# Kernel tuning notes

Measured on AMD Instinct MI355X. Metric: run time of the kernel, lower is better.

Reference implementation:

```python
import jax, jax.numpy as jnp
import numpy as np

LAMBDA_ENTROPY = 0.1
LAMBDA_REPULSION = 0.5
LAMBDA_INTER = 0.3
TEMPERATURE = 1.0
EPS = 1e-8


def setup_inputs() -> dict:
    key = jax.random.key(0)
    k1, k2 = jax.random.split(key)
    membership = jax.random.uniform(k1, (16384, 64, 32), dtype=jnp.float32)   # (N,F,K) soft bin assignments
    teacher_preds = jax.random.uniform(k2, (16384, 128), dtype=jnp.float32)   # (N,C)
    return {"membership": membership, "teacher_preds": teacher_preds}


def reference(membership, teacher_preds):
    N, F, K = membership.shape
    # --- weighted centroids per (feature, bin) ---
    bin_mass = membership.sum(axis=0) + EPS                       # (F,K)
    sum_weighted_y = jnp.einsum('nfk,nc->fkc', membership, teacher_preds)  # avoids (N,F,K,C)
    centroids = sum_weighted_y / bin_mass[..., None]              # (F,K,C)
    # --- weighted intra-bin variance: ||y_n - c_fk||^2 expanded, no (N,F,K,C) tensor ---
    y_sq = jnp.sum(teacher_preds * teacher_preds, axis=-1)        # (N,)
    c_sq = jnp.sum(centroids * centroids, axis=-1)                # (F,K)
    cross = jnp.einsum('nc,fkc->nfk', teacher_preds, centroids)   # (N,F,K)
    dist_sq = y_sq[:, None, None] + c_sq[None, :, :] - 2.0 * cross
    weighted_variance = jnp.sum(membership * dist_sq, axis=0) / bin_mass  # (F,K)
    loss_dispersion = weighted_variance.sum()
    # --- bin-occupancy entropy ---
    p_bins = bin_mass / N                                         # (F,K)
    loss_entropy = jnp.sum(p_bins * jnp.log(p_bins + EPS))
    # --- neighbor repulsion between adjacent bin centroids ---
    neighbor_dist = jnp.sum((centroids[:, :-1, :] - centroids[:, 1:, :]) ** 2, axis=-1)  # (F,K-1)
    loss_repulsion = jnp.sum(jnp.exp(-neighbor_dist / TEMPERATURE))
    # --- all-pairs inter-bin dispersion, batched over F (replaces python loop) ---
    dots = jnp.einsum('fkc,fjc->fkj', centroids, centroids)       # (F,K,K)
    pairwise = c_sq[:, :, None] + c_sq[:, None, :] - 2.0 * dots
    triu = jnp.triu(jnp.ones((K, K), dtype=centroids.dtype), k=1)  # strictly upper
    loss_inter = jnp.sum(jnp.exp(-pairwise / TEMPERATURE) * triu) / F
    total = (loss_dispersion
             + LAMBDA_ENTROPY * loss_entropy
             + LAMBDA_REPULSION * loss_repulsion
             + LAMBDA_INTER * loss_inter)
    return total, loss_dispersion, loss_entropy, loss_repulsion, loss_inter
```

## Files before the change

kernel.cpp:

```cpp
#include <hip/hip_runtime.h>
#include <math.h>

#define N_PTS   16384
#define F_DIM   64
#define K_BINS  32
#define C_DIM   128
#define FK      2048
#define NB32    (N_PTS / 32)
#define CW      132
#define EPS_F   1e-8f

typedef _Float16 f16x8 __attribute__((ext_vector_type(8)));
typedef float    f32x4 __attribute__((ext_vector_type(4)));

__global__ __launch_bounds__(256) void build_ybf_k(const float* __restrict__ Y,
                                                   _Float16* __restrict__ Ybf,
                                                   float* __restrict__ accs) {
    __shared__ __align__(16) float Yl[64][132];
    __shared__ float ysql[64];
    const int t  = threadIdx.x;
    if (blockIdx.x == 0 && t < 8) accs[t] = 0.0f;
    const int n0 = blockIdx.x * 64;
    const int nl = t >> 5;
    const int c4 = t & 31;
#pragma unroll
    for (int p = 0; p < 8; ++p) {
        const int n = p * 8 + nl;
        const float4 v = reinterpret_cast<const float4*>(Y + (size_t)(n0 + n) * C_DIM)[c4];
        reinterpret_cast<float4*>(Yl[n])[c4] = v;
        float sq = v.x * v.x + v.y * v.y + v.z * v.z + v.w * v.w;
#pragma unroll
        for (int m = 16; m >= 1; m >>= 1) sq += __shfl_xor(sq, m, 64);
        if (c4 == 0) ysql[n] = sq;
    }
    __syncthreads();
    for (int p = 0; p < 5; ++p) {
        const int s = t + p * 256;
        if (s < 1152) {
            const int nb2  = s / 576;
            const int r    = s % 576;
            const int ct   = r >> 6;
            const int l    = r & 63;
            const int quad = l >> 4, cl = l & 15;
            const int nloc = nb2 * 32 + quad * 8;
            f16x8 v;
            if (ct < 8) {
                const int c = ct * 16 + cl;
#pragma unroll
                for (int j = 0; j < 8; ++j) v[j] = (_Float16)Yl[nloc + j][c];
            } else if (cl == 0) {
#pragma unroll
                for (int j = 0; j < 8; ++j) v[j] = (_Float16)ysql[nloc + j];
            } else if (cl == 1) {
#pragma unroll
                for (int j = 0; j < 8; ++j) v[j] = (_Float16)1.0f;
            } else {
#pragma unroll
                for (int j = 0; j < 8; ++j) v[j] = (_Float16)0.0f;
            }
            const int nb = blockIdx.x * 2 + nb2;
            *reinterpret_cast<f16x8*>(Ybf + ((size_t)(ct * NB32 + nb) * 64 + l) * 8) = v;
        }
    }
}

__global__ __launch_bounds__(256) void gemm_k(const float* __restrict__ M,
                                              const _Float16* __restrict__ Ybf,
                                              float* __restrict__ wpart,
                                              int cn) {
    __shared__ __align__(16) float    At[2][2][32][32];
    __shared__ __align__(16) _Float16 Bb[2][2][9][512];
    const int t    = threadIdx.x;
    const int fk0  = blockIdx.x * 32;
    const int ch   = blockIdx.y;
    const int w    = t >> 6;
    const int g    = w >> 1;
    const int wl   = w & 1;
    const int l    = t & 63;
    const int quad = l >> 4;
    const int cl   = l & 15;
    const int n0   = ch * cn + g * (cn >> 1);
    const int nb0  = n0 >> 5;
    const int steps = cn >> 6;

    f32x4 acc[9] = {};

#define STAGE(s, par)                                                          \
    {                                                                          \
        const int nb_ = nb0 + (s);                                             \
        _Pragma("unroll")                                                      \
        for (int ct = wl; ct < 9; ct += 2) {                                   \
            const _Float16* g_ = Ybf + ((size_t)(ct * NB32 + nb_) * 64 + l) * 8; \
            __builtin_amdgcn_global_load_lds(                                  \
                (const __attribute__((address_space(1))) unsigned*)g_,         \
                (__attribute__((address_space(3))) unsigned*)&Bb[g][par][ct][0], \
                16, 0, 0);                                                     \
        }                                                                      \
        _Pragma("unroll")                                                      \
        for (int ii = 0; ii < 2; ++ii) {                                       \
            const int i = wl * 2 + ii;                                         \
            const float* gA = M + (size_t)(n0 + (s) * 32 + i * 8 + (l >> 3)) * FK \
                              + fk0 + (l & 7) * 4;                             \
            __builtin_amdgcn_global_load_lds(                                  \
                (const __attribute__((address_space(1))) unsigned*)gA,         \
                (__attribute__((address_space(3))) unsigned*)&At[g][par][i * 8][0], \
                16, 0, 0);                                                     \
        }                                                                      \
    }

    STAGE(0, 0);
    STAGE(1, 1);

    for (int s = 0; s < steps; s += 2) {
        __syncthreads();
        {
            f16x8 bf[9];
#pragma unroll
            for (int ct = 0; ct < 9; ++ct)
                bf[ct] = *reinterpret_cast<const f16x8*>(&Bb[g][0][ct][l * 8]);
            f16x8 af;
#pragma unroll
            for (int j = 0; j < 8; ++j)
                af[j] = (_Float16)At[g][0][quad * 8 + j][wl * 16 + cl];
            __syncthreads();
            if (s + 2 < steps) STAGE(s + 2, 0);
#pragma unroll
            for (int ct = 0; ct < 9; ++ct)
                acc[ct] = __builtin_amdgcn_mfma_f32_16x16x32_f16(af, bf[ct], acc[ct], 0, 0, 0);
        }
        __syncthreads();
        {
            f16x8 bf[9];
#pragma unroll
            for (int ct = 0; ct < 9; ++ct)
                bf[ct] = *reinterpret_cast<const f16x8*>(&Bb[g][1][ct][l * 8]);
            f16x8 af;
#pragma unroll
            for (int j = 0; j < 8; ++j)
                af[j] = (_Float16)At[g][1][quad * 8 + j][wl * 16 + cl];
            __syncthreads();
            if (s + 3 < steps) STAGE(s + 3, 1);
#pragma unroll
            for (int ct = 0; ct < 9; ++ct)
                acc[ct] = __builtin_amdgcn_mfma_f32_16x16x32_f16(af, bf[ct], acc[ct], 0, 0, 0);
        }
    }
#undef STAGE

    float* scr = reinterpret_cast<float*>(&Bb[0][0][0][0]);
    if (g == 1) {
#pragma unroll
        for (int ct = 0; ct < 9; ++ct)
#pragma unroll
            for (int r = 0; r < 4; ++r)
                scr[(wl * 16 + quad * 4 + r) * 144 + ct * 16 + cl] = acc[ct][r];
    }
    __syncthreads();
    if (g == 0) {
        float* wp = wpart + (size_t)ch * FK * CW;
#pragma unroll
        for (int ct = 0; ct < 9; ++ct) {
            const int c = ct * 16 + cl;
            if (c < CW) {
#pragma unroll
                for (int r = 0; r < 4; ++r) {
                    const int row = wl * 16 + quad * 4 + r;
                    const int fk  = fk0 + row;
                    wp[(size_t)fk * CW + c] = acc[ct][r] + scr[row * 144 + c];
                }
            }
        }
    }
}

__global__ __launch_bounds__(128) void reduce_w_k(const float* __restrict__ wpart,
                                                  float* __restrict__ W, int nchunk) {
    const int idx = blockIdx.x * 128 + threadIdx.x;
    const float4* src = reinterpret_cast<const float4*>(wpart);
    const size_t cs = (size_t)FK * CW / 4;
    float4 s0 = make_float4(0.f, 0.f, 0.f, 0.f), s1 = s0, s2 = s0, s3 = s0;
    int ch = 0;
    for (; ch + 3 < nchunk; ch += 4) {
        const float4 a = src[idx + (size_t)(ch + 0) * cs];
        const float4 b = src[idx + (size_t)(ch + 1) * cs];
        const float4 c = src[idx + (size_t)(ch + 2) * cs];
        const float4 d = src[idx + (size_t)(ch + 3) * cs];
        s0.x += a.x; s0.y += a.y; s0.z += a.z; s0.w += a.w;
        s1.x += b.x; s1.y += b.y; s1.z += b.z; s1.w += b.w;
        s2.x += c.x; s2.y += c.y; s2.z += c.z; s2.w += c.w;
        s3.x += d.x; s3.y += d.y; s3.z += d.z; s3.w += d.w;
    }
    for (; ch < nchunk; ++ch) {
        const float4 a = src[idx + (size_t)ch * cs];
        s0.x += a.x; s0.y += a.y; s0.z += a.z; s0.w += a.w;
    }
    float4 r;
    r.x = (s0.x + s1.x) + (s2.x + s3.x);
    r.y = (s0.y + s1.y) + (s2.y + s3.y);
    r.z = (s0.z + s1.z) + (s2.z + s3.z);
    r.w = (s0.w + s1.w) + (s2.w + s3.w);
    reinterpret_cast<float4*>(W)[idx] = r;
}

__global__ __launch_bounds__(256) void epilogue_k(const float* __restrict__ W,
                                                  float* __restrict__ accs,
                                                  float* __restrict__ out) {
    __shared__ __align__(16) float Wl[32][CW];
    __shared__ float Bv[32], Binv[32], S1v[32], csq[32];
    __shared__ float scr[32][8];
    __shared__ float4 red4[256];
    const int t = threadIdx.x;
    const int f = blockIdx.x;

    for (int e = t; e < 32 * 33; e += 256) {
        const int k = e / 33, c4 = e % 33;
        reinterpret_cast<float4*>(Wl[k])[c4] =
            reinterpret_cast<const float4*>(W + (size_t)(f * 32 + k) * CW)[c4];
    }
    __syncthreads();
    if (t < 32) {
        const float B = Wl[t][129] + EPS_F;
        Bv[t] = B; Binv[t] = 1.0f / B; S1v[t] = Wl[t][128];
    }
    __syncthreads();
    {
        const int k = t >> 3, g = t & 7;
        const float ib = Binv[k];
        float s = 0.f;
        for (int c = g * 16; c < g * 16 + 16; ++c) {
            const float v = Wl[k][c] * ib;
            Wl[k][c] = v;
            s = fmaf(v, v, s);
        }
        scr[k][g] = s;
    }
    __syncthreads();
    if (t < 32) {
        float s = 0.f;
#pragma unroll
        for (int g = 0; g < 8; ++g) s += scr[t][g];
        csq[t] = s;
    }
    __syncthreads();

    float my_disp = 0.f, my_ent = 0.f, my_rep = 0.f, my_inter = 0.f;
    if (t < 32) {
        my_disp = (S1v[t] - csq[t] * (Bv[t] + EPS_F)) * Binv[t];
        const float p = Bv[t] * (1.0f / (float)N_PTS);
        my_ent = p * logf(p + EPS_F);
    }
    {
        const int pr = t >> 3, g = t & 7;
        float s = 0.f;
        if (pr < 31) {
            for (int c = g * 16; c < g * 16 + 16; ++c) {
                const float d = Wl[pr][c] - Wl[pr + 1][c];
                s = fmaf(d, d, s);
            }
        }
        __syncthreads();
        scr[pr][g] = s;
    }
    __syncthreads();
    if (t < 31) {
        float d = 0.f;
#pragma unroll
        for (int g = 0; g < 8; ++g) d += scr[t][g];
        my_rep = expf(-d);
    }
#pragma unroll
    for (int s4 = 0; s4 < 4; ++s4) {
        const int slot = t + s4 * 256;
        const int k = slot >> 5, j = slot & 31;
        if (k < j) {
            float dot = 0.f;
            for (int c4 = 0; c4 < 32; ++c4) {
                const float4 a = reinterpret_cast<const float4*>(Wl[k])[c4];
                const float4 b = reinterpret_cast<const float4*>(Wl[j])[c4];
                dot = fmaf(a.x, b.x, dot); dot = fmaf(a.y, b.y, dot);
                dot = fmaf(a.z, b.z, dot); dot = fmaf(a.w, b.w, dot);
            }
            my_inter += expf(-(csq[k] + csq[j] - 2.0f * dot));
        }
    }
    red4[t] = make_float4(my_disp, my_ent, my_rep, my_inter);
    __syncthreads();
    for (int off = 128; off >= 1; off >>= 1) {
        if (t < off) {
            const float4 a = red4[t], b = red4[t + off];
            red4[t] = make_float4(a.x + b.x, a.y + b.y, a.z + b.z, a.w + b.w);
        }
        __syncthreads();
    }
    if (t == 0) {
        atomicAdd(accs + 0, red4[0].x);
        atomicAdd(accs + 1, red4[0].y);
        atomicAdd(accs + 2, red4[0].z);
        atomicAdd(accs + 3, red4[0].w);
        __threadfence();
        const unsigned prev = __hip_atomic_fetch_add(
            reinterpret_cast<unsigned*>(accs + 4), 1u,
            __ATOMIC_ACQ_REL, __HIP_MEMORY_SCOPE_AGENT);
        if (prev == (unsigned)(F_DIM - 1)) {
            const float disp = __hip_atomic_load(accs + 0, __ATOMIC_RELAXED, __HIP_MEMORY_SCOPE_AGENT);
            const float ent  = __hip_atomic_load(accs + 1, __ATOMIC_RELAXED, __HIP_MEMORY_SCOPE_AGENT);
            const float rep  = __hip_atomic_load(accs + 2, __ATOMIC_RELAXED, __HIP_MEMORY_SCOPE_AGENT);
            const float inter = __hip_atomic_load(accs + 3, __ATOMIC_RELAXED, __HIP_MEMORY_SCOPE_AGENT)
                                * (1.0f / (float)F_DIM);
            out[0] = disp + 0.1f * ent + 0.5f * rep + 0.3f * inter;
            out[1] = disp;
            out[2] = ent;
            out[3] = rep;
            out[4] = inter;
        }
    }
}

extern "C" void kernel_launch(void* const* d_in, const int* in_sizes, int n_in,
                              void* d_out, int out_size, void* d_ws, size_t ws_size,
                              hipStream_t stream) {
    const float* M = (const float*)d_in[0];
    const float* Y = (const float*)d_in[1];
    float* out = (float*)d_out;
    char*  ws  = (char*)d_ws;

    const size_t ybfBytes = (size_t)9 * NB32 * 64 * 8 * sizeof(_Float16);
    const size_t wBytes   = (size_t)FK * CW * sizeof(float);

    _Float16* Ybf   = (_Float16*)ws;
    float*    W     = (float*)(ws + ybfBytes);
    float*    accs  = (float*)(ws + ybfBytes + wBytes);
    float*    wpart = (float*)(ws + ybfBytes + wBytes + 1024);

    const size_t used = ybfBytes + wBytes + 1024;
    int nchunk = 16;
    while (nchunk > 1 && used + (size_t)nchunk * wBytes > ws_size) nchunk >>= 1;
    const int cn = N_PTS / nchunk;

    build_ybf_k<<<dim3(N_PTS / 64), dim3(256), 0, stream>>>(Y, Ybf, accs);
    gemm_k<<<dim3(64, nchunk), dim3(256), 0, stream>>>(M, Ybf, wpart, cn);
    reduce_w_k<<<dim3(FK * CW / 4 / 128), dim3(128), 0, stream>>>(wpart, W, nchunk);
    epilogue_k<<<dim3(F_DIM), dim3(256), 0, stream>>>(W, accs, out);
}
```

Baseline: 237.7 us.

## Pre-transpose membership into fp16 MFMA fragment layout in a separate kernel

Adds a build_mt_k pass that reads the fp32 membership tensor once, converts it to fp16 and stores it in the per-lane MFMA A-fragment order. The GEMM then loads A fragments straight into registers with one 16-byte load instead of staging fp32 tiles in LDS and converting per element. The cost is an extra full pass over M (128MB read plus 64MB fp16 write) and 64MB more workspace. The gain depends on whether the GEMM was bound by LDS conversion rather than HBM bandwidth.

Result: slower. 253.0 us (+6.4%).

```diff
diff --git a/kernel.cpp b/kernel.cpp
--- a/kernel.cpp
+++ b/kernel.cpp
@@ -64,11 +64,47 @@
     }
 }
 
-__global__ __launch_bounds__(256) void gemm_k(const float* __restrict__ M,
+__global__ __launch_bounds__(256) void build_mt_k(const float* __restrict__ M,
+                                                  _Float16* __restrict__ Mt) {
+    __shared__ __align__(16) float Lt[32][260];
+    const int t    = threadIdx.x;
+    const int nb   = blockIdx.x;
+    const int half = blockIdx.y;
+    const int n0   = nb * 32;
+#pragma unroll
+    for (int pass = 0; pass < 4; ++pass) {
+        const int fkbase = (half * 4 + pass) * 256;
+        __syncthreads();
+#pragma unroll
+        for (int i = 0; i < 8; ++i) {
+            const int idx = t + i * 256;
+            const int row = idx >> 6;
+            const int c4  = idx & 63;
+            const float4 v = reinterpret_cast<const float4*>(
+                M + (size_t)(n0 + row) * FK + fkbase)[c4];
+            reinterpret_cast<float4*>(&Lt[row][0])[c4] = v;
+        }
+        __syncthreads();
+#pragma unroll
+        for (int k2 = 0; k2 < 4; ++k2) {
+            const int s   = t + k2 * 256;
+            const int fbl = s >> 6;
+            const int l   = s & 63;
+            const int quad = l >> 4, cl = l & 15;
+            f16x8 v;
+#pragma unroll
+            for (int j = 0; j < 8; ++j)
+                v[j] = (_Float16)Lt[quad * 8 + j][fbl * 16 + cl];
+            const int fb = (half * 4 + pass) * 16 + fbl;
+            *reinterpret_cast<f16x8*>(Mt + ((size_t)(fb * NB32 + nb) * 64 + l) * 8) = v;
+        }
+    }
+}
+
+__global__ __launch_bounds__(256) void gemm_k(const _Float16* __restrict__ Mt,
                                               const _Float16* __restrict__ Ybf,
                                               float* __restrict__ wpart,
                                               int cn) {
-    __shared__ __align__(16) float    At[2][2][32][32];
     __shared__ __align__(16) _Float16 Bb[2][2][9][512];
     const int t    = threadIdx.x;
     const int fk0  = blockIdx.x * 32;
@@ -82,8 +118,11 @@
     const int n0   = ch * cn + g * (cn >> 1);
     const int nb0  = n0 >> 5;
     const int steps = cn >> 6;
+    const int fb   = blockIdx.x * 2 + wl;
+    const _Float16* mtp = Mt + ((size_t)fb * NB32 * 64 + l) * 8;
 
     f32x4 acc[9] = {};
+    f16x8 ar[2];
 
 #define STAGE(s, par)                                                          \
     {                                                                          \
@@ -96,20 +135,12 @@
                 (__attribute__((address_space(3))) unsigned*)&Bb[g][par][ct][0], \
                 16, 0, 0);                                                     \
         }                                                                      \
-        _Pragma("unroll")                                                      \
-        for (int ii = 0; ii < 2; ++ii) {                                       \
-            const int i = wl * 2 + ii;                                         \
-            const float* gA = M + (size_t)(n0 + (s) * 32 + i * 8 + (l >> 3)) * FK \
-                              + fk0 + (l & 7) * 4;                             \
-            __builtin_amdgcn_global_load_lds(                                  \
-                (const __attribute__((address_space(1))) unsigned*)gA,         \
-                (__attribute__((address_space(3))) unsigned*)&At[g][par][i * 8][0], \
-                16, 0, 0);                                                     \
-        }                                                                      \
-    }
-
-    STAGE(0, 0);
-    STAGE(1, 1);
+    }
+#define LOADA(buf, s)                                                          \
+    ar[buf] = *reinterpret_cast<const f16x8*>(mtp + (size_t)(nb0 + (s)) * 512);
+
+    STAGE(0, 0); LOADA(0, 0);
+    STAGE(1, 1); LOADA(1, 1);
 
     for (int s = 0; s < steps; s += 2) {
         __syncthreads();
@@ -118,12 +149,9 @@
 #pragma unroll
             for (int ct = 0; ct < 9; ++ct)
                 bf[ct] = *reinterpret_cast<const f16x8*>(&Bb[g][0][ct][l * 8]);
-            f16x8 af;
-#pragma unroll
-            for (int j = 0; j < 8; ++j)
-                af[j] = (_Float16)At[g][0][quad * 8 + j][wl * 16 + cl];
+            const f16x8 af = ar[0];
             __syncthreads();
-            if (s + 2 < steps) STAGE(s + 2, 0);
+            if (s + 2 < steps) { STAGE(s + 2, 0); LOADA(0, s + 2); }
 #pragma unroll
             for (int ct = 0; ct < 9; ++ct)
                 acc[ct] = __builtin_amdgcn_mfma_f32_16x16x32_f16(af, bf[ct], acc[ct], 0, 0, 0);
@@ -134,18 +162,16 @@
 #pragma unroll
             for (int ct = 0; ct < 9; ++ct)
                 bf[ct] = *reinterpret_cast<const f16x8*>(&Bb[g][1][ct][l * 8]);
-            f16x8 af;
-#pragma unroll
-            for (int j = 0; j < 8; ++j)
-                af[j] = (_Float16)At[g][1][quad * 8 + j][wl * 16 + cl];
+            const f16x8 af = ar[1];
             __syncthreads();
-            if (s + 3 < steps) STAGE(s + 3, 1);
+            if (s + 3 < steps) { STAGE(s + 3, 1); LOADA(1, s + 3); }
 #pragma unroll
             for (int ct = 0; ct < 9; ++ct)
                 acc[ct] = __builtin_amdgcn_mfma_f32_16x16x32_f16(af, bf[ct], acc[ct], 0, 0, 0);
         }
     }
 #undef STAGE
+#undef LOADA
 
     float* scr = reinterpret_cast<float*>(&Bb[0][0][0][0]);
     if (g == 1) {
@@ -325,20 +351,23 @@
     char*  ws  = (char*)d_ws;
 
     const size_t ybfBytes = (size_t)9 * NB32 * 64 * 8 * sizeof(_Float16);
+    const size_t mtBytes  = (size_t)FK * N_PTS * sizeof(_Float16);
     const size_t wBytes   = (size_t)FK * CW * sizeof(float);
 
     _Float16* Ybf   = (_Float16*)ws;
-    float*    W     = (float*)(ws + ybfBytes);
-    float*    accs  = (float*)(ws + ybfBytes + wBytes);
-    float*    wpart = (float*)(ws + ybfBytes + wBytes + 1024);
-
-    const size_t used = ybfBytes + wBytes + 1024;
+    _Float16* Mt    = (_Float16*)(ws + ybfBytes);
+    float*    W     = (float*)(ws + ybfBytes + mtBytes);
+    float*    accs  = (float*)(ws + ybfBytes + mtBytes + wBytes);
+    float*    wpart = (float*)(ws + ybfBytes + mtBytes + wBytes + 1024);
+
+    const size_t used = ybfBytes + mtBytes + wBytes + 1024;
     int nchunk = 16;
     while (nchunk > 1 && used + (size_t)nchunk * wBytes > ws_size) nchunk >>= 1;
     const int cn = N_PTS / nchunk;
 
     build_ybf_k<<<dim3(N_PTS / 64), dim3(256), 0, stream>>>(Y, Ybf, accs);
-    gemm_k<<<dim3(64, nchunk), dim3(256), 0, stream>>>(M, Ybf, wpart, cn);
+    build_mt_k<<<dim3(NB32, 2), dim3(256), 0, stream>>>(M, Mt);
+    gemm_k<<<dim3(64, nchunk), dim3(256), 0, stream>>>(Mt, Ybf, wpart, cn);
     reduce_w_k<<<dim3(FK * CW / 4 / 128), dim3(128), 0, stream>>>(wpart, W, nchunk);
     epilogue_k<<<dim3(F_DIM), dim3(256), 0, stream>>>(W, accs, out);
 }
```

## Widen GEMM block tile to 128 FK rows and drop intra-block N split

Applied to the files above, without the earlier changes.

The GEMM block now covers 128 fk rows with each wave computing two 16-row MFMA tiles, so every staged Ybf tile is reused across four times as many membership rows. The two-group split over N inside a block and its LDS reduction are removed, and N parallelism moves to more chunks (64 instead of 16), with an occupancy hint of 3 blocks per CU. This cuts redundant B-tile loads and the in-block reduction. In exchange, the partial-sum buffer and the reduce pass grow with the chunk count, and register pressure per wave rises.

New measurement: 236.2 us. About the same (-0.7%).

```diff
diff --git a/kernel.cpp b/kernel.cpp
--- a/kernel.cpp
+++ b/kernel.cpp
@@ -64,46 +64,44 @@
     }
 }
 
-__global__ __launch_bounds__(256) void gemm_k(const float* __restrict__ M,
-                                              const _Float16* __restrict__ Ybf,
-                                              float* __restrict__ wpart,
-                                              int cn) {
-    __shared__ __align__(16) float    At[2][2][32][32];
-    __shared__ __align__(16) _Float16 Bb[2][2][9][512];
+__global__ __launch_bounds__(256, 3) void gemm_k(const float* __restrict__ M,
+                                                 const _Float16* __restrict__ Ybf,
+                                                 float* __restrict__ wpart,
+                                                 int cn) {
+    __shared__ __align__(16) float    At[2][32][128];
+    __shared__ __align__(16) _Float16 Bb[2][9][512];
     const int t    = threadIdx.x;
-    const int fk0  = blockIdx.x * 32;
+    const int fk0  = blockIdx.x * 128;
     const int ch   = blockIdx.y;
     const int w    = t >> 6;
-    const int g    = w >> 1;
-    const int wl   = w & 1;
     const int l    = t & 63;
     const int quad = l >> 4;
     const int cl   = l & 15;
-    const int n0   = ch * cn + g * (cn >> 1);
+    const int n0   = ch * cn;
     const int nb0  = n0 >> 5;
-    const int steps = cn >> 6;
-
-    f32x4 acc[9] = {};
+    const int steps = cn >> 5;
+
+    f32x4 acc[2][9] = {};
 
 #define STAGE(s, par)                                                          \
     {                                                                          \
         const int nb_ = nb0 + (s);                                             \
         _Pragma("unroll")                                                      \
-        for (int ct = wl; ct < 9; ct += 2) {                                   \
+        for (int ct = w; ct < 9; ct += 4) {                                    \
             const _Float16* g_ = Ybf + ((size_t)(ct * NB32 + nb_) * 64 + l) * 8; \
             __builtin_amdgcn_global_load_lds(                                  \
                 (const __attribute__((address_space(1))) unsigned*)g_,         \
-                (__attribute__((address_space(3))) unsigned*)&Bb[g][par][ct][0], \
+                (__attribute__((address_space(3))) unsigned*)&Bb[par][ct][0],  \
                 16, 0, 0);                                                     \
         }                                                                      \
         _Pragma("unroll")                                                      \
-        for (int ii = 0; ii < 2; ++ii) {                                       \
-            const int i = wl * 2 + ii;                                         \
-            const float* gA = M + (size_t)(n0 + (s) * 32 + i * 8 + (l >> 3)) * FK \
-                              + fk0 + (l & 7) * 4;                             \
+        for (int i = 0; i < 4; ++i) {                                          \
+            const int row = w * 8 + i * 2 + (l >> 5);                          \
+            const float* gA = M + (size_t)(n0 + (s) * 32 + row) * FK           \
+                              + fk0 + (l & 31) * 4;                            \
             __builtin_amdgcn_global_load_lds(                                  \
                 (const __attribute__((address_space(1))) unsigned*)gA,         \
-                (__attribute__((address_space(3))) unsigned*)&At[g][par][i * 8][0], \
+                (__attribute__((address_space(3))) unsigned*)&At[par][w * 8 + i * 2][0], \
                 16, 0, 0);                                                     \
         }                                                                      \
     }
@@ -117,56 +115,55 @@
             f16x8 bf[9];
 #pragma unroll
             for (int ct = 0; ct < 9; ++ct)
-                bf[ct] = *reinterpret_cast<const f16x8*>(&Bb[g][0][ct][l * 8]);
-            f16x8 af;
-#pragma unroll
-            for (int j = 0; j < 8; ++j)
-                af[j] = (_Float16)At[g][0][quad * 8 + j][wl * 16 + cl];
+                bf[ct] = *reinterpret_cast<const f16x8*>(&Bb[0][ct][l * 8]);
+            f16x8 af0, af1;
+#pragma unroll
+            for (int j = 0; j < 8; ++j) {
+                af0[j] = (_Float16)At[0][quad * 8 + j][w * 32 + cl];
+                af1[j] = (_Float16)At[0][quad * 8 + j][w * 32 + 16 + cl];
+            }
             __syncthreads();
             if (s + 2 < steps) STAGE(s + 2, 0);
 #pragma unroll
-            for (int ct = 0; ct < 9; ++ct)
-                acc[ct] = __builtin_amdgcn_mfma_f32_16x16x32_f16(af, bf[ct], acc[ct], 0, 0, 0);
+            for (int ct = 0; ct < 9; ++ct) {
+                acc[0][ct] = __builtin_amdgcn_mfma_f32_16x16x32_f16(af0, bf[ct], acc[0][ct], 0, 0, 0);
+                acc[1][ct] = __builtin_amdgcn_mfma_f32_16x16x32_f16(af1, bf[ct], acc[1][ct], 0, 0, 0);
+            }
         }
         __syncthreads();
         {
             f16x8 bf[9];
 #pragma unroll
             for (int ct = 0; ct < 9; ++ct)
-                bf[ct] = *reinterpret_cast<const f16x8*>(&Bb[g][1][ct][l * 8]);
-            f16x8 af;
-#pragma unroll
-            for (int j = 0; j < 8; ++j)
-                af[j] = (_Float16)At[g][1][quad * 8 + j][wl * 16 + cl];
+                bf[ct] = *reinterpret_cast<const f16x8*>(&Bb[1][ct][l * 8]);
+            f16x8 af0, af1;
+#pragma unroll
+            for (int j = 0; j < 8; ++j) {
+                af0[j] = (_Float16)At[1][quad * 8 + j][w * 32 + cl];
+                af1[j] = (_Float16)At[1][quad * 8 + j][w * 32 + 16 + cl];
+            }
             __syncthreads();
             if (s + 3 < steps) STAGE(s + 3, 1);
 #pragma unroll
-            for (int ct = 0; ct < 9; ++ct)
-                acc[ct] = __builtin_amdgcn_mfma_f32_16x16x32_f16(af, bf[ct], acc[ct], 0, 0, 0);
+            for (int ct = 0; ct < 9; ++ct) {
+                acc[0][ct] = __builtin_amdgcn_mfma_f32_16x16x32_f16(af0, bf[ct], acc[0][ct], 0, 0, 0);
+                acc[1][ct] = __builtin_amdgcn_mfma_f32_16x16x32_f16(af1, bf[ct], acc[1][ct], 0, 0, 0);
+            }
         }
     }
 #undef STAGE
 
-    float* scr = reinterpret_cast<float*>(&Bb[0][0][0][0]);
-    if (g == 1) {
-#pragma unroll
-        for (int ct = 0; ct < 9; ++ct)
-#pragma unroll
-            for (int r = 0; r < 4; ++r)
-                scr[(wl * 16 + quad * 4 + r) * 144 + ct * 16 + cl] = acc[ct][r];
-    }
-    __syncthreads();
-    if (g == 0) {
-        float* wp = wpart + (size_t)ch * FK * CW;
+    float* wp = wpart + (size_t)ch * FK * CW;
+#pragma unroll
+    for (int f = 0; f < 2; ++f) {
 #pragma unroll
         for (int ct = 0; ct < 9; ++ct) {
             const int c = ct * 16 + cl;
             if (c < CW) {
 #pragma unroll
                 for (int r = 0; r < 4; ++r) {
-                    const int row = wl * 16 + quad * 4 + r;
-                    const int fk  = fk0 + row;
-                    wp[(size_t)fk * CW + c] = acc[ct][r] + scr[row * 144 + c];
+                    const int fk = fk0 + w * 32 + f * 16 + quad * 4 + r;
+                    wp[(size_t)fk * CW + c] = acc[f][ct][r];
                 }
             }
         }
@@ -333,12 +330,12 @@
     float*    wpart = (float*)(ws + ybfBytes + wBytes + 1024);
 
     const size_t used = ybfBytes + wBytes + 1024;
-    int nchunk = 16;
+    int nchunk = 64;
     while (nchunk > 1 && used + (size_t)nchunk * wBytes > ws_size) nchunk >>= 1;
     const int cn = N_PTS / nchunk;
 
     build_ybf_k<<<dim3(N_PTS / 64), dim3(256), 0, stream>>>(Y, Ybf, accs);
-    gemm_k<<<dim3(64, nchunk), dim3(256), 0, stream>>>(M, Ybf, wpart, cn);
+    gemm_k<<<dim3(16, nchunk), dim3(256), 0, stream>>>(M, Ybf, wpart, cn);
     reduce_w_k<<<dim3(FK * CW / 4 / 128), dim3(128), 0, stream>>>(wpart, W, nchunk);
     epilogue_k<<<dim3(F_DIM), dim3(256), 0, stream>>>(W, accs, out);
 }
```
